# Performance work log

Measured on AMD Instinct MI355X. Metric: run time of the kernel, lower is better.

Reference implementation:

```python
import jax, jax.numpy as jnp
import numpy as np

B, N, K = 4, 8192, 16
FEAT = 512
GRID = 45
M = GRID * GRID


def _p(key, shape, scale=0.05):
    return jax.random.normal(key, shape, dtype=jnp.float32) * scale


def setup_inputs() -> dict:
    key = jax.random.key(0)
    ks = jax.random.split(key, 40)
    inp = {"pts": jax.random.normal(ks[0], (B, N, 3), dtype=jnp.float32)}
    specs = {
        "w1": (64, 12), "b1": (64,), "w2": (64, 64), "b2": (64,), "w3": (64, 64), "b3": (64,),
        "g1a": (64, 64), "g1ab": (64,), "g1b": (128, 64), "g1bb": (128,),
        "g2a": (128, 128), "g2ab": (128,), "g2b": (1024, 128), "g2bb": (1024,),
        "m1": (FEAT, 1024), "m1b": (FEAT,), "m2": (FEAT, FEAT), "m2b": (FEAT,),
        "f1a": (FEAT, FEAT + 2), "f1ab": (FEAT,), "f1b": (FEAT, FEAT), "f1bb": (FEAT,), "f1c": (3, FEAT), "f1cb": (3,),
        "f2a": (FEAT, FEAT + 3), "f2ab": (FEAT,), "f2b": (FEAT, FEAT), "f2bb": (FEAT,), "f2c": (3, FEAT), "f2cb": (3,),
    }
    for i, (name, shp) in enumerate(specs.items()):
        inp[name] = _p(ks[i + 1], shp)
    return inp


def conv1x1(x, w, b):
    # x: (B,C,N), w: (Cout,Cin), b: (Cout,)
    return jnp.einsum('bcn,oc->bon', x, w) + b[None, :, None]


def knn_idx(x, k):
    # x: (B,C,N) -> neighbor indices (B,N,k) by smallest squared distance (self included)
    xt = jnp.swapaxes(x, 1, 2)                      # (B,N,C)
    sq = jnp.sum(xt * xt, axis=-1)                  # (B,N)
    inner = jnp.einsum('bnc,bmc->bnm', xt, xt)      # (B,N,N)
    neg_d2 = 2.0 * inner - sq[:, :, None] - sq[:, None, :]
    return jax.lax.top_k(neg_d2, k)[1]


def gather_nbrs(feats_t, idx):
    # feats_t: (B,N,C), idx: (B,N,k) -> (B,N,k,C)
    return jax.vmap(lambda f, i: f[i])(feats_t, idx)


def local_maxpool(x, idx):
    # x: (B,C,N) -> (B,C,N) max over k neighbors
    nb = gather_nbrs(jnp.swapaxes(x, 1, 2), idx)    # (B,N,k,C)
    return jnp.swapaxes(jnp.max(nb, axis=2), 1, 2)


def local_cov(pts_t, idx):
    # pts_t: (B,3,N) -> (B,12,N): coords + outer product of first two neighbors
    p = jnp.swapaxes(pts_t, 1, 2)                   # (B,N,3)
    nb = gather_nbrs(p, idx)                        # (B,N,k,3)
    outer = nb[:, :, 0, :, None] * nb[:, :, 1, None, :]   # (B,N,3,3)
    feat = jnp.concatenate([p, outer.reshape(p.shape[0], p.shape[1], 9)], axis=-1)
    return jnp.swapaxes(feat, 1, 2)


def _forward(pts, w1, b1, w2, b2, w3, b3, g1a, g1ab, g1b, g1bb, g2a, g2ab, g2b, g2bb,
             m1, m1b, m2, m2b, f1a, f1ab, f1b, f1bb, f1c, f1cb, f2a, f2ab, f2b, f2bb, f2c, f2cb):
    relu = jax.nn.relu
    pts_t = jnp.swapaxes(pts, 1, 2)                 # (B,3,N)
    # ---- encoder ----
    idx = knn_idx(pts_t, K)
    x = local_cov(pts_t, idx)                       # (B,12,N)
    x = relu(conv1x1(x, w1, b1))
    x = relu(conv1x1(x, w2, b2))
    x = relu(conv1x1(x, w3, b3))                    # (B,64,N)
    idx = knn_idx(x, K)
    g = local_maxpool(x, idx)
    g = conv1x1(relu(conv1x1(g, g1a, g1ab)), g1b, g1bb)   # (B,128,N)
    idx = knn_idx(g, K)
    h = local_maxpool(g, idx)
    h = conv1x1(relu(conv1x1(h, g2a, g2ab)), g2b, g2bb)   # (B,1024,N)
    glob = jnp.max(h, axis=2, keepdims=True)        # (B,1024,1)
    code = conv1x1(relu(conv1x1(glob, m1, m1b)), m2, m2b)  # (B,FEAT,1)
    # ---- decoder ----
    Bs = code.shape[0]
    cw = jnp.broadcast_to(code, (Bs, FEAT, M))
    lin = jnp.linspace(-0.3, 0.3, GRID, dtype=jnp.float32)
    gx, gy = jnp.meshgrid(lin, lin, indexing='ij')
    grid = jnp.stack([gx.ravel(), gy.ravel()], axis=0)     # (2,M)
    grid = jnp.broadcast_to(grid[None], (Bs, 2, M))

    def fold(points, wa, ba, wb, bb, wc, bc):
        y = jnp.concatenate([cw, points], axis=1)
        y = relu(conv1x1(y, wa, ba))
        y = relu(conv1x1(y, wb, bb))
        return conv1x1(y, wc, bc)                    # (B,3,M)

    mid = fold(grid, f1a, f1ab, f1b, f1bb, f1c, f1cb)
    rec = fold(mid, f2a, f2ab, f2b, f2bb, f2c, f2cb)
    return jnp.swapaxes(rec, 1, 2)                   # (B,M,3)


def reference(pts, w1, b1, w2, b2, w3, b3, g1a, g1ab, g1b, g1bb, g2a, g2ab, g2b, g2bb,
              m1, m1b, m2, m2b, f1a, f1ab, f1b, f1bb, f1c, f1cb, f2a, f2ab, f2b, f2bb, f2c, f2cb):
    return _forward(pts, w1, b1, w2, b2, w3, b3, g1a, g1ab, g1b, g1bb, g2a, g2ab, g2b, g2bb,
                    m1, m1b, m2, m2b, f1a, f1ab, f1b, f1bb, f1c, f1cb, f2a, f2ab, f2b, f2bb, f2c, f2cb)
```

## Files before the change

### kernel.cpp

```cpp
#include <hip/hip_runtime.h>
#include <stdint.h>

#define B_ 4
#define N_ 8192
#define K_ 16
#define FEAT_ 512
#define GRID_ 45
#define M_ (GRID_*GRID_)

typedef unsigned long long ull;
typedef __bf16 bf16x8 __attribute__((ext_vector_type(8)));
typedef float f32x16 __attribute__((ext_vector_type(16)));


__device__ __forceinline__ unsigned int fmap(float f){
  unsigned int u = __float_as_uint(f);
  return (u & 0x80000000u) ? ~u : (u | 0x80000000u);
}
__device__ __forceinline__ float funmap(unsigned int u){
  return (u & 0x80000000u) ? __uint_as_float(u ^ 0x80000000u) : __uint_as_float(~u);
}

__device__ __forceinline__ void ins16(ull (&d)[16], ull k){
  if (k < d[15]){
    bool c[16];
#pragma unroll
    for (int s = 0; s < 16; ++s) c[s] = k < d[s];
#pragma unroll
    for (int s = 15; s >= 1; --s) d[s] = c[s-1] ? d[s-1] : (c[s] ? k : d[s]);
    if (c[0]) d[0] = k;
  }
}

__device__ __forceinline__ void ins16b(unsigned (&dk)[16], unsigned (&di)[16],
                                       unsigned k, unsigned id){
  if (k < dk[15]){
    bool c[16];
#pragma unroll
    for (int s = 0; s < 16; ++s) c[s] = k < dk[s];
#pragma unroll
    for (int s = 15; s >= 1; --s){
      dk[s] = c[s-1] ? dk[s-1] : (c[s] ? k  : dk[s]);
      di[s] = c[s-1] ? di[s-1] : (c[s] ? id : di[s]);
    }
    if (c[0]){ dk[0] = k; di[0] = id; }
  }
}

#define GLDS16(l, g) __builtin_amdgcn_global_load_lds((const __attribute__((address_space(1))) void*)(g), (__attribute__((address_space(3))) void*)(l), 16, 0, 0)
#define GLDS4(l, g)  __builtin_amdgcn_global_load_lds((const __attribute__((address_space(1))) void*)(g), (__attribute__((address_space(3))) void*)(l), 4, 0, 0)

#define KEY_INF 0xFF800000FFFFFFFFull

__global__ void k_init(unsigned int* glob){
  int i = blockIdx.x*256 + threadIdx.x;
  if (i < B_*1024) glob[i] = 0x007FFFFFu;
}

__global__ __launch_bounds__(256) void k_nn1(const float* __restrict__ pts,
                                             unsigned long long* __restrict__ nn64){
  __shared__ float sp[2048*3];
  int b = blockIdx.z, s = blockIdx.y;
  int c0 = s*2048;
  const float* P = pts + (size_t)b*N_*3;
  for (int i = threadIdx.x; i < 2048*3; i += 256) sp[i] = P[c0*3 + i];
  __syncthreads();
  int n = blockIdx.x*256 + threadIdx.x;
  float qx = P[n*3], qy = P[n*3+1], qz = P[n*3+2];
  float best = 1e30f; int bi = 0;
  for (int j = 0; j < 2048; ++j){
    float dx = qx - sp[j*3], dy = qy - sp[j*3+1], dz = qz - sp[j*3+2];
    float d2 = fmaf(dx,dx, fmaf(dy,dy, dz*dz));
    int cj = c0 + j;
    if (d2 < best && cj != n){ best = d2; bi = cj; }
  }
  unsigned long long key = ((unsigned long long)__float_as_uint(best) << 32) | (unsigned int)bi;
  atomicMin(&nn64[(size_t)b*N_ + n], key);
}

__global__ __launch_bounds__(256) void k_cov_mlp(const float* __restrict__ pts,
    const unsigned long long* __restrict__ nn64,
    const float* __restrict__ w1, const float* __restrict__ b1,
    const float* __restrict__ w2, const float* __restrict__ b2,
    const float* __restrict__ w3, const float* __restrict__ b3,
    float* __restrict__ xout){
  __shared__ __align__(16) float W1t[12*64];
  __shared__ __align__(16) float W2t[64*64];
  __shared__ __align__(16) float W3t[64*64];
  __shared__ float B1[64], B2[64], B3[64];
  __shared__ __align__(16) float x0[64][12];
  __shared__ __align__(16) float h1[64][64];
  __shared__ __align__(16) float h2[64][64];
  int b = blockIdx.y; int n0 = blockIdx.x*64; int tid = threadIdx.x;
  for (int i = tid; i < 12*64; i += 256){ int o = i % 64, ci = i / 64; W1t[i] = w1[o*12 + ci]; }
  for (int i = tid; i < 64*64; i += 256){ int o = i % 64, ci = i / 64; W2t[i] = w2[o*64 + ci]; W3t[i] = w3[o*64 + ci]; }
  if (tid < 64){ B1[tid]=b1[tid]; B2[tid]=b2[tid]; B3[tid]=b3[tid]; }
  {
    int p = tid % 64, cg = tid / 64;
    int n = n0 + p;
    const float* P = pts + ((size_t)b*N_ + n)*3;
    int nb = (int)(nn64[(size_t)b*N_ + n] & 0xFFFFFFFFull);
    const float* Q = pts + ((size_t)b*N_ + nb)*3;
    if (cg == 0){ x0[p][0]=P[0]; x0[p][1]=P[1]; x0[p][2]=P[2]; }
    else { int i = cg-1; float pi = P[i];
      x0[p][3+i*3+0]=pi*Q[0]; x0[p][3+i*3+1]=pi*Q[1]; x0[p][3+i*3+2]=pi*Q[2]; }
  }
  __syncthreads();
  { int o = tid % 64, pg = tid / 64;
    for (int p = pg; p < 64; p += 4){
      float acc = B1[o];
#pragma unroll
      for (int ci = 0; ci < 12; ++ci) acc = fmaf(W1t[ci*64+o], x0[p][ci], acc);
      h1[p][o] = fmaxf(acc, 0.f);
    } }
  __syncthreads();
  { int o = tid % 64, pg = tid / 64;
    for (int p = pg; p < 64; p += 4){
      float acc = B2[o];
#pragma unroll
      for (int ci = 0; ci < 64; ++ci) acc = fmaf(W2t[ci*64+o], h1[p][ci], acc);
      h2[p][o] = fmaxf(acc, 0.f);
    } }
  __syncthreads();
  { int o = tid % 64, pg = tid / 64;
    for (int p = pg; p < 64; p += 4){
      float acc = B3[o];
#pragma unroll
      for (int ci = 0; ci < 64; ++ci) acc = fmaf(W3t[ci*64+o], h2[p][ci], acc);
      xout[((size_t)b*N_ + n0 + p)*64 + o] = fmaxf(acc, 0.f);
    } }
}

template<int KF>
__global__ __launch_bounds__(256) void k_prep4(const float* __restrict__ f,
    unsigned short* __restrict__ T, float* __restrict__ cc){
  int b = blockIdx.y; int n = blockIdx.x*256 + threadIdx.x;
  const float* src = f + ((size_t)b*N_ + n)*(KF*16);
  char* Tb = (char*)T;
  float ss = 0.f;
#pragma unroll
  for (int kf = 0; kf < KF; ++kf){
    float v[16];
#pragma unroll
    for (int c4 = 0; c4 < 4; ++c4){
      float4 t4 = *(const float4*)&src[kf*16 + c4*4];
      v[c4*4]=t4.x; v[c4*4+1]=t4.y; v[c4*4+2]=t4.z; v[c4*4+3]=t4.w;
    }
    unsigned short hs[16], ls[16];
#pragma unroll
    for (int c = 0; c < 16; ++c){
      float x = v[c];
      ss = fmaf(x, x, ss);
      __bf16 h = (__bf16)x;
      __bf16 l = (__bf16)(x - (float)h);
      hs[c] = __builtin_bit_cast(unsigned short, h);
      ls[c] = __builtin_bit_cast(unsigned short, l);
    }
    size_t base = ((((size_t)b*KF + kf)*2)*2)*(size_t)(N_*16) + (size_t)n*16;
    const size_t HS = (size_t)N_*16;
    const size_t PS = 2*HS;
    *(uint4*)(Tb + base)            = *(uint4*)&hs[0];
    *(uint4*)(Tb + base + HS)       = *(uint4*)&hs[8];
    *(uint4*)(Tb + base + PS)       = *(uint4*)&ls[0];
    *(uint4*)(Tb + base + PS + HS)  = *(uint4*)&ls[8];
  }
  cc[(size_t)b*N_ + n] = ss;
}

template<int KF, int MW, int S>
__global__ __launch_bounds__(256, MW) void k_knnF(const unsigned short* __restrict__ T,
    const float* __restrict__ ccg, ull* __restrict__ qkeys){
  extern __shared__ char smem[];
  constexpr int NT = (N_/S)/64;
  char* As = smem;
  char* Cs = smem + KF*4096;

  const int tid = threadIdx.x, lane = tid & 63, wid = tid >> 6;
  const int hi = lane >> 5, l31 = lane & 31;
  const int b = blockIdx.z, sp = blockIdx.y, q0 = blockIdx.x*128;
  const int c0 = sp*(N_/S);
  const char* Tb = (const char*)T;
  const size_t HS = (size_t)N_*16, PS = 2*HS, KS = 4*HS;
  const size_t Bb = (size_t)b*KF*KS;
  const float* ccb = ccg + (size_t)b*N_;

  const int q = q0 + wid*32 + l31;
  bf16x8 qh[KF], ql[KF];
#pragma unroll
  for (int kf = 0; kf < KF; ++kf){
    size_t o = Bb + kf*KS + hi*HS + (size_t)q*16;
    qh[kf] = *(const bf16x8*)(Tb + o);
    ql[kf] = *(const bf16x8*)(Tb + o + PS);
  }

  unsigned dk[16], di[16];
#pragma unroll
  for (int t = 0; t < 16; ++t){ dk[t] = 0xFFFFFFFFu; di[t] = 0xFFFFFFFFu; }
  float kapf = __builtin_inff();

  auto stage = [&](int t0){
#pragma unroll
    for (int si = 0; si < KF; ++si){
      int s = wid + 4*si;
      int kf = s >> 2, pl = (s >> 1) & 1, h = s & 1;
      GLDS16(As + s*1024,
             Tb + Bb + kf*KS + pl*PS + h*HS + (size_t)(c0 + t0)*16);
    }
    if (wid == 0) GLDS4(Cs, (const char*)(ccb + c0 + t0));
  };

  for (int t = 0; t < NT; ++t){
    const int t0 = t*64;
    __syncthreads();
    stage(t0);
    asm volatile("s_waitcnt vmcnt(0)" ::: "memory");
    __syncthreads();

    const char* Ab = As + hi*1024 + l31*16;
    const float* cct = (const float*)Cs;
#pragma unroll
    for (int i = 0; i < 2; ++i){
      f32x16 acc = (f32x16)(0.f);
#pragma unroll
      for (int kf = 0; kf < KF; ++kf){
        bf16x8 ah = *(const bf16x8*)(Ab + kf*4096 + i*512);
        bf16x8 al = *(const bf16x8*)(Ab + kf*4096 + 2048 + i*512);
        acc = __builtin_amdgcn_mfma_f32_32x32x16_bf16(ah, qh[kf], acc, 0, 0, 0);
        acc = __builtin_amdgcn_mfma_f32_32x32x16_bf16(ah, ql[kf], acc, 0, 0, 0);
        acc = __builtin_amdgcn_mfma_f32_32x32x16_bf16(al, qh[kf], acc, 0, 0, 0);
      }
#pragma unroll
      for (int rq = 0; rq < 4; ++rq){
        float4 c4 = *(const float4*)(cct + i*32 + 4*hi + 8*rq);
        int rowb = c0 + t0 + i*32 + 4*hi + 8*rq;
        float v0 = fmaf(-2.f, acc[rq*4+0], c4.x);
        float v1 = fmaf(-2.f, acc[rq*4+1], c4.y);
        float v2 = fmaf(-2.f, acc[rq*4+2], c4.z);
        float v3 = fmaf(-2.f, acc[rq*4+3], c4.w);
        if (fminf(fminf(v0, v1), fminf(v2, v3)) < kapf){
          if (v0 < kapf) ins16b(dk, di, fmap(v0), (unsigned)(rowb+0));
          if (v1 < kapf) ins16b(dk, di, fmap(v1), (unsigned)(rowb+1));
          if (v2 < kapf) ins16b(dk, di, fmap(v2), (unsigned)(rowb+2));
          if (v3 < kapf) ins16b(dk, di, fmap(v3), (unsigned)(rowb+3));
          unsigned kk = dk[15];
          kapf = (kk >= 0xFF800000u) ? __builtin_inff() : funmap(kk);
        }
      }
    }
  }
  ull* op = qkeys + (((size_t)((size_t)b*N_ + q)*S + sp)*2 + hi)*16;
#pragma unroll
  for (int t = 0; t < 16; ++t) op[t] = ((ull)dk[t] << 32) | di[t];
}

template<int S>
__global__ void k_sel(const ull* __restrict__ qkeys, int* __restrict__ idxout){
  int i = blockIdx.x*256 + threadIdx.x;
  if (i >= B_*N_) return;
  ull best[16];
#pragma unroll
  for (int t = 0; t < 16; ++t) best[t] = KEY_INF;
  const ull* kp = qkeys + (size_t)i*(S*32);
  for (int t = 0; t < S*32; ++t) ins16(best, kp[t]);
  int* op = idxout + (size_t)i*16;
#pragma unroll
  for (int t = 0; t < 16; ++t) op[t] = (int)(best[t] & 0xffffffffu);
}

__global__ __launch_bounds__(256) void k_gpool_mlp(const float* __restrict__ x,
    const int* __restrict__ idx,
    const float* __restrict__ g1a, const float* __restrict__ g1ab,
    const float* __restrict__ g1b, const float* __restrict__ g1bb,
    float* __restrict__ gout){
  __shared__ __align__(16) float Wt1[64*64];
  __shared__ __align__(16) float Wt2[64*128];
  __shared__ float Ba[64], Bb[128];
  __shared__ __align__(16) float m[64][64];
  __shared__ __align__(16) float r[64][64];
  int b = blockIdx.y; int n0 = blockIdx.x*64; int tid = threadIdx.x;
  for (int i = tid; i < 64*64; i += 256){ int o = i%64, ci = i/64; Wt1[i] = g1a[o*64+ci]; }
  for (int i = tid; i < 64*128; i += 256){ int o = i%128, ci = i/128; Wt2[i] = g1b[o*64+ci]; }
  if (tid < 64) Ba[tid] = g1ab[tid];
  if (tid < 128) Bb[tid] = g1bb[tid];
  { int p = tid/4, cg = tid%4; int n = n0 + p;
    const int* ip = idx + ((size_t)b*N_ + n)*16;
    float mm[16];
#pragma unroll
    for (int u = 0; u < 16; ++u) mm[u] = -1e30f;
    for (int k = 0; k < 16; ++k){
      int nb = ip[k];
      const float4* src = (const float4*)(x + ((size_t)b*N_ + nb)*64 + cg*16);
#pragma unroll
      for (int u = 0; u < 4; ++u){
        float4 v = src[u];
        mm[4*u  ] = fmaxf(mm[4*u  ], v.x); mm[4*u+1] = fmaxf(mm[4*u+1], v.y);
        mm[4*u+2] = fmaxf(mm[4*u+2], v.z); mm[4*u+3] = fmaxf(mm[4*u+3], v.w);
      }
    }
#pragma unroll
    for (int u = 0; u < 16; ++u) m[p][cg*16+u] = mm[u];
  }
  __syncthreads();
  { int o = tid%64, pg = tid/64;
    float acc[16];
#pragma unroll
    for (int u = 0; u < 16; ++u) acc[u] = Ba[o];
    for (int ci = 0; ci < 64; ci += 4){
      float w0 = Wt1[ci*64+o], w1_ = Wt1[(ci+1)*64+o], w2_ = Wt1[(ci+2)*64+o], w3_ = Wt1[(ci+3)*64+o];
#pragma unroll
      for (int u = 0; u < 16; ++u){
        float4 mv = *(const float4*)&m[pg*16+u][ci];
        acc[u] = fmaf(w0, mv.x, acc[u]); acc[u] = fmaf(w1_, mv.y, acc[u]);
        acc[u] = fmaf(w2_, mv.z, acc[u]); acc[u] = fmaf(w3_, mv.w, acc[u]);
      }
    }
#pragma unroll
    for (int u = 0; u < 16; ++u) r[pg*16+u][o] = fmaxf(acc[u], 0.f);
  }
  __syncthreads();
  { int o = tid%128, pg = tid/128;
    float acc[32];
#pragma unroll
    for (int u = 0; u < 32; ++u) acc[u] = Bb[o];
    for (int ci = 0; ci < 64; ci += 4){
      float w0 = Wt2[ci*128+o], w1_ = Wt2[(ci+1)*128+o], w2_ = Wt2[(ci+2)*128+o], w3_ = Wt2[(ci+3)*128+o];
#pragma unroll
      for (int u = 0; u < 32; ++u){
        float4 rv = *(const float4*)&r[pg*32+u][ci];
        acc[u] = fmaf(w0, rv.x, acc[u]); acc[u] = fmaf(w1_, rv.y, acc[u]);
        acc[u] = fmaf(w2_, rv.z, acc[u]); acc[u] = fmaf(w3_, rv.w, acc[u]);
      }
    }
#pragma unroll
    for (int u = 0; u < 32; ++u)
      gout[((size_t)b*N_ + n0 + pg*32 + u)*128 + o] = acc[u];
  }
}

__global__ __launch_bounds__(256) void k_hpool_max(const float* __restrict__ g,
    const int* __restrict__ idx,
    const float* __restrict__ g2a, const float* __restrict__ g2ab,
    const float* __restrict__ g2b, const float* __restrict__ g2bb,
    unsigned int* __restrict__ glob){
  __shared__ __align__(16) float m[32][128];
  __shared__ __align__(16) float t[32][128];
  int b = blockIdx.y; int n0 = blockIdx.x*32; int tid = threadIdx.x;
  { int p = tid/8, cg = tid%8; int n = n0+p;
    const int* ip = idx + ((size_t)b*N_+n)*16;
    float mm[16];
#pragma unroll
    for (int u = 0; u < 16; ++u) mm[u] = -1e30f;
    for (int k = 0; k < 16; ++k){
      int nb = ip[k];
      const float4* src = (const float4*)(g + ((size_t)b*N_+nb)*128 + cg*16);
#pragma unroll
      for (int u = 0; u < 4; ++u){
        float4 v = src[u];
        mm[4*u  ] = fmaxf(mm[4*u  ], v.x); mm[4*u+1] = fmaxf(mm[4*u+1], v.y);
        mm[4*u+2] = fmaxf(mm[4*u+2], v.z); mm[4*u+3] = fmaxf(mm[4*u+3], v.w);
      }
    }
#pragma unroll
    for (int u = 0; u < 16; ++u) m[p][cg*16+u] = mm[u];
  }
  __syncthreads();
  { int o = tid%128, pg = tid/128;
    float acc[16];
#pragma unroll
    for (int u = 0; u < 16; ++u) acc[u] = g2ab[o];
    const float4* wrow = (const float4*)(g2a + (size_t)o*128);
    for (int c4 = 0; c4 < 32; ++c4){
      float4 wv = wrow[c4];
#pragma unroll
      for (int u = 0; u < 16; ++u){
        float4 mv = *(const float4*)&m[pg*16+u][c4*4];
        acc[u] = fmaf(wv.x,mv.x,acc[u]); acc[u] = fmaf(wv.y,mv.y,acc[u]);
        acc[u] = fmaf(wv.z,mv.z,acc[u]); acc[u] = fmaf(wv.w,mv.w,acc[u]);
      }
    }
#pragma unroll
    for (int u = 0; u < 16; ++u) t[pg*16+u][o] = fmaxf(acc[u], 0.f);
  }
  __syncthreads();
  for (int oc = 0; oc < 4; ++oc){
    int o = oc*256 + tid;
    const float4* wrow = (const float4*)(g2b + (size_t)o*128);
    float acc[32];
#pragma unroll
    for (int u = 0; u < 32; ++u) acc[u] = 0.f;
    for (int c4 = 0; c4 < 32; ++c4){
      float4 wv = wrow[c4];
#pragma unroll
      for (int u = 0; u < 32; ++u){
        float4 tv = *(const float4*)&t[u][c4*4];
        acc[u] = fmaf(wv.x,tv.x,acc[u]); acc[u] = fmaf(wv.y,tv.y,acc[u]);
        acc[u] = fmaf(wv.z,tv.z,acc[u]); acc[u] = fmaf(wv.w,tv.w,acc[u]);
      }
    }
    float bias = g2bb[o];
    float mx = -1e30f;
#pragma unroll
    for (int u = 0; u < 32; ++u) mx = fmaxf(mx, acc[u] + bias);
    atomicMax(&glob[b*1024 + o], fmap(mx));
  }
}

__global__ __launch_bounds__(512) void k_code(const unsigned int* __restrict__ glob,
    const float* __restrict__ m1, const float* __restrict__ m1b,
    const float* __restrict__ m2, const float* __restrict__ m2b,
    const float* __restrict__ f1a, const float* __restrict__ f1ab,
    const float* __restrict__ f2a, const float* __restrict__ f2ab,
    float* __restrict__ base1, float* __restrict__ base2){
  __shared__ __align__(16) float gl_s[1024];
  __shared__ __align__(16) float hid_s[512];
  __shared__ __align__(16) float code_s[512];
  int b = blockIdx.x; int tid = threadIdx.x;
  for (int i = tid; i < 1024; i += 512) gl_s[i] = funmap(glob[b*1024+i]);
  __syncthreads();
  { float acc = m1b[tid];
    const float4* wr = (const float4*)(m1 + (size_t)tid*1024);
    for (int c4 = 0; c4 < 256; ++c4){ float4 wv = wr[c4]; float4 gv = *(const float4*)&gl_s[c4*4];
      acc = fmaf(wv.x,gv.x,acc); acc = fmaf(wv.y,gv.y,acc);
      acc = fmaf(wv.z,gv.z,acc); acc = fmaf(wv.w,gv.w,acc); }
    hid_s[tid] = fmaxf(acc, 0.f);
  }
  __syncthreads();
  { float acc = m2b[tid];
    const float4* wr = (const float4*)(m2 + (size_t)tid*512);
    for (int c4 = 0; c4 < 128; ++c4){ float4 wv = wr[c4]; float4 hv = *(const float4*)&hid_s[c4*4];
      acc = fmaf(wv.x,hv.x,acc); acc = fmaf(wv.y,hv.y,acc);
      acc = fmaf(wv.z,hv.z,acc); acc = fmaf(wv.w,hv.w,acc); }
    code_s[tid] = acc;
  }
  __syncthreads();
  { float acc = f1ab[tid];
    const float* wr = f1a + (size_t)tid*514;
    for (int c = 0; c < 512; ++c) acc = fmaf(wr[c], code_s[c], acc);
    base1[b*512 + tid] = acc;
  }
  { float acc = f2ab[tid];
    const float* wr = f2a + (size_t)tid*515;
    for (int c = 0; c < 512; ++c) acc = fmaf(wr[c], code_s[c], acc);
    base2[b*512 + tid] = acc;
  }
}

template<int NIN>
__global__ __launch_bounds__(256) void k_fold(const float* __restrict__ base,
    const float* __restrict__ fa,
    const float* __restrict__ fb, const float* __restrict__ fbb,
    const float* __restrict__ fc, const float* __restrict__ fcb,
    const float* __restrict__ pin, float* __restrict__ pout){
  __shared__ __align__(16) float y1[32][512];
  __shared__ __align__(16) float y2[32][516];
  __shared__ float pcoord[32][NIN];
  int b = blockIdx.y; int m0 = blockIdx.x*32; int tid = threadIdx.x;
  if (tid < 32*NIN){
    int p = tid / NIN, c = tid % NIN;
    int mm = min(m0 + p, M_-1);
    float v;
    if (NIN == 2){
      const float step = 0.6f/44.f;
      int ii = (c == 0) ? (mm/GRID_) : (mm%GRID_);
      v = -0.3f + step*ii;
    } else {
      v = pin[((size_t)b*M_ + mm)*3 + c];
    }
    pcoord[p][c] = v;
  }
  __syncthreads();
  const int stride_a = 512 + NIN;
  for (int rep = 0; rep < 2; ++rep){
    int o = rep*256 + tid;
    float av[NIN];
#pragma unroll
    for (int c = 0; c < NIN; ++c) av[c] = fa[(size_t)o*stride_a + 512 + c];
    float bv = base[b*512 + o];
    for (int p = 0; p < 32; ++p){
      float acc = bv;
#pragma unroll
      for (int c = 0; c < NIN; ++c) acc = fmaf(av[c], pcoord[p][c], acc);
      y1[p][o] = fmaxf(acc, 0.f);
    }
  }
  __syncthreads();
  for (int rep = 0; rep < 2; ++rep){
    int o2 = rep*256 + tid;
    const float* wr = fb + (size_t)o2*512;
    float acc[32];
#pragma unroll
    for (int u = 0; u < 32; ++u) acc[u] = 0.f;
    for (int c4 = 0; c4 < 128; ++c4){
      float4 wv = *(const float4*)&wr[c4*4];
#pragma unroll
      for (int u = 0; u < 32; ++u){
        float4 yv = *(const float4*)&y1[u][c4*4];
        acc[u] = fmaf(wv.x,yv.x,acc[u]); acc[u] = fmaf(wv.y,yv.y,acc[u]);
        acc[u] = fmaf(wv.z,yv.z,acc[u]); acc[u] = fmaf(wv.w,yv.w,acc[u]);
      }
    }
    float bias = fbb[o2];
#pragma unroll
    for (int u = 0; u < 32; ++u) y2[u][o2] = fmaxf(acc[u] + bias, 0.f);
  }
  __syncthreads();
  if (tid < 96){
    int p = tid / 3, c = tid % 3;
    const float* wr = fc + (size_t)c*512;
    float acc = fcb[c];
    for (int o4 = 0; o4 < 128; ++o4){
      float4 wv = *(const float4*)&wr[o4*4];
      float4 yv = *(const float4*)&y2[p][o4*4];
      acc = fmaf(wv.x,yv.x,acc); acc = fmaf(wv.y,yv.y,acc);
      acc = fmaf(wv.z,yv.z,acc); acc = fmaf(wv.w,yv.w,acc);
    }
    int mm = m0 + p;
    if (mm < M_) pout[((size_t)b*M_ + mm)*3 + c] = acc;
  }
}

extern "C" void kernel_launch(void* const* d_in, const int* in_sizes, int n_in,
                              void* d_out, int out_size, void* d_ws, size_t ws_size,
                              hipStream_t stream){
  const float* pts  = (const float*)d_in[0];
  const float* w1   = (const float*)d_in[1];  const float* b1   = (const float*)d_in[2];
  const float* w2   = (const float*)d_in[3];  const float* b2   = (const float*)d_in[4];
  const float* w3   = (const float*)d_in[5];  const float* b3   = (const float*)d_in[6];
  const float* g1a  = (const float*)d_in[7];  const float* g1ab = (const float*)d_in[8];
  const float* g1b  = (const float*)d_in[9];  const float* g1bb = (const float*)d_in[10];
  const float* g2a  = (const float*)d_in[11]; const float* g2ab = (const float*)d_in[12];
  const float* g2b  = (const float*)d_in[13]; const float* g2bb = (const float*)d_in[14];
  const float* m1   = (const float*)d_in[15]; const float* m1b  = (const float*)d_in[16];
  const float* m2   = (const float*)d_in[17]; const float* m2b  = (const float*)d_in[18];
  const float* f1a  = (const float*)d_in[19]; const float* f1ab = (const float*)d_in[20];
  const float* f1b  = (const float*)d_in[21]; const float* f1bb = (const float*)d_in[22];
  const float* f1c  = (const float*)d_in[23]; const float* f1cb = (const float*)d_in[24];
  const float* f2a  = (const float*)d_in[25]; const float* f2ab = (const float*)d_in[26];
  const float* f2b  = (const float*)d_in[27]; const float* f2bb = (const float*)d_in[28];
  const float* f2c  = (const float*)d_in[29]; const float* f2cb = (const float*)d_in[30];
  float* out = (float*)d_out;

  char* w = (char*)d_ws;
  auto alloc = [&](size_t bytes){ char* p = w; w += (bytes + 255) & ~(size_t)255; return p; };
  unsigned long long* nn64 = (unsigned long long*)alloc((size_t)B_*N_*8);
  float* x    = (float*)alloc((size_t)B_*N_*64*4);
  float* g    = (float*)alloc((size_t)B_*N_*128*4);
  unsigned short* T64  = (unsigned short*)alloc((size_t)B_*4*4*N_*16);
  unsigned short* T128 = (unsigned short*)alloc((size_t)B_*8*4*N_*16);
  float* ccf  = (float*)alloc((size_t)B_*N_*4);
  int*   idx  = (int*)alloc((size_t)B_*N_*16*4);
  ull*   qkeys = (ull*)alloc((size_t)B_*N_*4*2*16*8);
  unsigned int* glob = (unsigned int*)alloc((size_t)B_*1024*4);
  float* base1 = (float*)alloc((size_t)B_*512*4);
  float* base2 = (float*)alloc((size_t)B_*512*4);
  float* mid   = (float*)alloc((size_t)B_*M_*3*4);
  (void)ws_size; (void)in_sizes; (void)n_in; (void)out_size;

  const int SMEM4 = 4*4096 + 256;
  const int SMEM8 = 8*4096 + 256;
  hipFuncSetAttribute((const void*)k_knnF<4,4,4>, hipFuncAttributeMaxDynamicSharedMemorySize, SMEM4);
  hipFuncSetAttribute((const void*)k_knnF<8,3,4>, hipFuncAttributeMaxDynamicSharedMemorySize, SMEM8);

  hipMemsetAsync(nn64, 0xFF, (size_t)B_*N_*8, stream);
  k_init<<<dim3((B_*1024+255)/256), 256, 0, stream>>>(glob);
  k_nn1<<<dim3(N_/256, 4, B_), 256, 0, stream>>>(pts, nn64);
  k_cov_mlp<<<dim3(N_/64, B_), 256, 0, stream>>>(pts, nn64, w1,b1,w2,b2,w3,b3, x);

  k_prep4<4><<<dim3(N_/256, B_), 256, 0, stream>>>(x, T64, ccf);
  k_knnF<4,4,4><<<dim3(N_/128, 4, B_), 256, SMEM4, stream>>>(T64, ccf, qkeys);
  k_sel<4><<<dim3(B_*N_/256), 256, 0, stream>>>(qkeys, idx);

  k_gpool_mlp<<<dim3(N_/64, B_), 256, 0, stream>>>(x, idx, g1a,g1ab,g1b,g1bb, g);

  k_prep4<8><<<dim3(N_/256, B_), 256, 0, stream>>>(g, T128, ccf);
  k_knnF<8,3,4><<<dim3(N_/128, 4, B_), 256, SMEM8, stream>>>(T128, ccf, qkeys);
  k_sel<4><<<dim3(B_*N_/256), 256, 0, stream>>>(qkeys, idx);

  k_hpool_max<<<dim3(N_/32, B_), 256, 0, stream>>>(g, idx, g2a,g2ab,g2b,g2bb, glob);
  k_code<<<dim3(B_), 512, 0, stream>>>(glob, m1,m1b,m2,m2b, f1a,f1ab, f2a,f2ab, base1, base2);
  k_fold<2><<<dim3((M_+31)/32, B_), 256, 0, stream>>>(base1, f1a, f1b, f1bb, f1c, f1cb, nullptr, mid);
  k_fold<3><<<dim3((M_+31)/32, B_), 256, 0, stream>>>(base2, f2a, f2b, f2bb, f2c, f2cb, mid, out);
}
```

Before: 1.743 ms.

## Buffer kNN candidates in LDS and drain in wave-uniform batches

```diff
diff --git a/kernel.cpp b/kernel.cpp
--- a/kernel.cpp
+++ b/kernel.cpp
@@ -34,7 +34,7 @@
 
 __device__ __forceinline__ void ins16b(unsigned (&dk)[16], unsigned (&di)[16],
                                        unsigned k, unsigned id){
-  if (k < dk[15]){
+  if (k < dk[16-1]){
     bool c[16];
 #pragma unroll
     for (int s = 0; s < 16; ++s) c[s] = k < dk[s];
@@ -174,6 +174,8 @@
   constexpr int NT = (N_/S)/64;
   char* As = smem;
   char* Cs = smem + KF*4096;
+  unsigned* Pk = (unsigned*)(smem + KF*4096 + 256);
+  unsigned* Pi = Pk + 8*256;
 
   const int tid = threadIdx.x, lane = tid & 63, wid = tid >> 6;
   const int hi = lane >> 5, l31 = lane & 31;
@@ -197,6 +199,16 @@
 #pragma unroll
   for (int t = 0; t < 16; ++t){ dk[t] = 0xFFFFFFFFu; di[t] = 0xFFFFFFFFu; }
   float kapf = __builtin_inff();
+  int cnt = 0;
+
+  auto drain = [&](){
+#pragma unroll
+    for (int t = 0; t < 8; ++t)
+      if (t < cnt) ins16b(dk, di, Pk[t*256 + tid], Pi[t*256 + tid]);
+    cnt = 0;
+    unsigned kk = dk[15];
+    kapf = (kk >= 0xFF800000u) ? __builtin_inff() : funmap(kk);
+  };
 
   auto stage = [&](int t0){
 #pragma unroll
@@ -229,25 +241,39 @@
         acc = __builtin_amdgcn_mfma_f32_32x32x16_bf16(ah, ql[kf], acc, 0, 0, 0);
         acc = __builtin_amdgcn_mfma_f32_32x32x16_bf16(al, qh[kf], acc, 0, 0, 0);
       }
-#pragma unroll
-      for (int rq = 0; rq < 4; ++rq){
-        float4 c4 = *(const float4*)(cct + i*32 + 4*hi + 8*rq);
-        int rowb = c0 + t0 + i*32 + 4*hi + 8*rq;
-        float v0 = fmaf(-2.f, acc[rq*4+0], c4.x);
-        float v1 = fmaf(-2.f, acc[rq*4+1], c4.y);
-        float v2 = fmaf(-2.f, acc[rq*4+2], c4.z);
-        float v3 = fmaf(-2.f, acc[rq*4+3], c4.w);
-        if (fminf(fminf(v0, v1), fminf(v2, v3)) < kapf){
-          if (v0 < kapf) ins16b(dk, di, fmap(v0), (unsigned)(rowb+0));
-          if (v1 < kapf) ins16b(dk, di, fmap(v1), (unsigned)(rowb+1));
-          if (v2 < kapf) ins16b(dk, di, fmap(v2), (unsigned)(rowb+2));
-          if (v3 < kapf) ins16b(dk, di, fmap(v3), (unsigned)(rowb+3));
-          unsigned kk = dk[15];
-          kapf = (kk >= 0xFF800000u) ? __builtin_inff() : funmap(kk);
+      if (t == 0){
+#pragma unroll
+        for (int rq = 0; rq < 4; ++rq){
+          float4 c4 = *(const float4*)(cct + i*32 + 4*hi + 8*rq);
+          int rowb = c0 + i*32 + 4*hi + 8*rq;
+          ins16b(dk, di, fmap(fmaf(-2.f, acc[rq*4+0], c4.x)), (unsigned)(rowb+0));
+          ins16b(dk, di, fmap(fmaf(-2.f, acc[rq*4+1], c4.y)), (unsigned)(rowb+1));
+          ins16b(dk, di, fmap(fmaf(-2.f, acc[rq*4+2], c4.z)), (unsigned)(rowb+2));
+          ins16b(dk, di, fmap(fmaf(-2.f, acc[rq*4+3], c4.w)), (unsigned)(rowb+3));
         }
-      }
-    }
-  }
+        unsigned kk = dk[15];
+        kapf = (kk >= 0xFF800000u) ? __builtin_inff() : funmap(kk);
+      } else {
+#pragma unroll
+        for (int rq = 0; rq < 4; ++rq){
+          float4 c4 = *(const float4*)(cct + i*32 + 4*hi + 8*rq);
+          int rowb = c0 + t0 + i*32 + 4*hi + 8*rq;
+          float v0 = fmaf(-2.f, acc[rq*4+0], c4.x);
+          float v1 = fmaf(-2.f, acc[rq*4+1], c4.y);
+          float v2 = fmaf(-2.f, acc[rq*4+2], c4.z);
+          float v3 = fmaf(-2.f, acc[rq*4+3], c4.w);
+          if (fminf(fminf(v0, v1), fminf(v2, v3)) < kapf){
+            if (v0 < kapf){ Pk[cnt*256+tid] = fmap(v0); Pi[cnt*256+tid] = (unsigned)(rowb+0); ++cnt; }
+            if (v1 < kapf){ Pk[cnt*256+tid] = fmap(v1); Pi[cnt*256+tid] = (unsigned)(rowb+1); ++cnt; }
+            if (v2 < kapf){ Pk[cnt*256+tid] = fmap(v2); Pi[cnt*256+tid] = (unsigned)(rowb+2); ++cnt; }
+            if (v3 < kapf){ Pk[cnt*256+tid] = fmap(v3); Pi[cnt*256+tid] = (unsigned)(rowb+3); ++cnt; }
+          }
+          if (__any(cnt >= 5)) drain();
+        }
+      }
+    }
+  }
+  drain();
   ull* op = qkeys + (((size_t)((size_t)b*N_ + q)*S + sp)*2 + hi)*16;
 #pragma unroll
   for (int t = 0; t < 16; ++t) op[t] = ((ull)dk[t] << 32) | di[t];
@@ -556,8 +582,9 @@
   float* mid   = (float*)alloc((size_t)B_*M_*3*4);
   (void)ws_size; (void)in_sizes; (void)n_in; (void)out_size;
 
-  const int SMEM4 = 4*4096 + 256;
-  const int SMEM8 = 8*4096 + 256;
+  const int QB = 2*8*256*4;
+  const int SMEM4 = 4*4096 + 256 + QB;
+  const int SMEM8 = 8*4096 + 256 + QB;
   hipFuncSetAttribute((const void*)k_knnF<4,4,4>, hipFuncAttributeMaxDynamicSharedMemorySize, SMEM4);
   hipFuncSetAttribute((const void*)k_knnF<8,3,4>, hipFuncAttributeMaxDynamicSharedMemorySize, SMEM8);
 
```

Measured after the change: 1.872 ms. 1.07x slower.
